# Performance work log

Hardware: AMD Instinct MI355X
Metric: run time of the kernel (lower is better)

## Reference

```python
import jax, jax.numpy as jnp
import numpy as np

B, S, H, P, T = 8, 2048, 1024, 256, 4
EPS = 1e-12


def setup_inputs() -> dict:
    key = jax.random.key(0)
    ks = jax.random.split(key, 12)
    sd = 0.02
    return {
        "hidden_states": jax.random.normal(ks[0], (B, S, H), jnp.float32),
        "input_tensor": jax.random.normal(ks[1], (B, S, H), jnp.float32),
        "attention_mask": jnp.zeros((B, 1, 1, S), jnp.float32),
        "dense_W": jax.random.normal(ks[2], (H, H), jnp.float32) * sd,
        "dense_b": jnp.zeros((H,), jnp.float32),
        "pal_W1": jax.random.normal(ks[3], (T, H, P), jnp.float32) * sd,  # H2L per task
        "pal_b1": jnp.zeros((T, P), jnp.float32),
        "pal_W2": jax.random.normal(ks[4], (T, P, H), jnp.float32) * sd,  # L2H per task
        "pal_b2": jnp.zeros((T, H), jnp.float32),
        "enc_W": jax.random.normal(ks[5], (H,), jnp.float32) * sd,  # Linear(H,1)
        "enc_b": jnp.zeros((), jnp.float32),
        "sel_W": jax.random.normal(ks[6], (T, H), jnp.float32) * sd,  # Linear(H,T)
        "sel_b": jnp.zeros((T,), jnp.float32),
        "ln_g": jnp.ones((H,), jnp.float32),
        "ln_b": jnp.zeros((H,), jnp.float32),
    }


def reference(hidden_states, input_tensor, attention_mask, dense_W, dense_b,
              pal_W1, pal_b1, pal_W2, pal_b2, enc_W, enc_b, sel_W, sel_b,
              ln_g, ln_b):
    # dense projection (dropout p=0 -> identity)
    h = jnp.einsum('bsh,hk->bsk', hidden_states, dense_W) + dense_b  # [B,S,H]

    # per-task PAL adapters: H -> P -> H, stacked over T
    low = jnp.einsum('bsh,thp->btsp', h, pal_W1) + pal_b1[:, None, :]   # [B,T,S,P]
    task_specific = jnp.einsum('btsp,tph->btsh', low, pal_W2) + pal_b2[:, None, :]  # [B,T,S,H]

    # token-level gating: softmax over sequence of (encoder logits + additive mask)
    task_logits = jnp.einsum('bsh,h->bs', h, enc_W) + enc_b            # [B,S]
    task_weights = jax.nn.softmax(task_logits + attention_mask.reshape(B, S), axis=-1)
    task_vector = jnp.einsum('bs,bsh->bh', task_weights, h)            # [B,H]

    # task selector distribution and weighted combine over task branches
    task_distribution = jax.nn.softmax(task_vector @ sel_W.T + sel_b, axis=-1)  # [B,T]
    summed = jnp.einsum('btsh,bt->bsh', task_specific, task_distribution)       # [B,S,H]

    # residual + LayerNorm (eps=1e-12)
    x = h + input_tensor + summed
    mu = x.mean(-1, keepdims=True)
    var = ((x - mu) ** 2).mean(-1, keepdims=True)
    return ln_g * (x - mu) / jnp.sqrt(var + EPS) + ln_b
```

## Files before the change

### kernel.cpp

```cpp
#include <hip/hip_runtime.h>
#include <stdint.h>

#define DEVI __device__ __forceinline__

typedef __attribute__((ext_vector_type(8))) short s8v;
typedef __attribute__((ext_vector_type(4))) float f4v;
typedef unsigned short u16;

DEVI float bf2f(u16 u) { union { uint32_t i; float f; } c; c.i = ((uint32_t)u) << 16; return c.f; }
DEVI u16 f2bf(float f) {
  union { float f; uint32_t u; } c; c.f = f;
  uint32_t u = c.u;
  u += 0x7fffu + ((u >> 16) & 1u);
  return (u16)(u >> 16);
}

DEVI void gld16(const void* g, void* l) {
  auto gp = reinterpret_cast<const __attribute__((address_space(1))) void*>(reinterpret_cast<uintptr_t>(g));
  auto lp = reinterpret_cast<__attribute__((address_space(3))) void*>(reinterpret_cast<uintptr_t>(l));
  __builtin_amdgcn_global_load_lds(gp, lp, 16, 0, 0);
}

DEVI float wredsum(float v) {
  #pragma unroll
  for (int o = 32; o; o >>= 1) v += __shfl_xor(v, o);
  return v;
}

#define MFMA16(a, b, c) __builtin_amdgcn_mfma_f32_16x16x32_bf16((a), (b), (c), 0, 0, 0)

__global__ void cvt_f32_bf16(const float4* __restrict__ in, ushort4* __restrict__ out) {
  int i = blockIdx.x * 256 + threadIdx.x;
  float4 v = in[i];
  ushort4 o;
  o.x = f2bf(v.x); o.y = f2bf(v.y); o.z = f2bf(v.z); o.w = f2bf(v.w);
  out[i] = o;
}

__global__ void transpose_cvt(const float* __restrict__ in, u16* __restrict__ out, int R, int C) {
  __shared__ float t[32][33];
  in  += (size_t)blockIdx.z * R * C;
  out += (size_t)blockIdx.z * R * C;
  int r0 = blockIdx.y * 32, c0 = blockIdx.x * 32;
  int tx = threadIdx.x, ty = threadIdx.y;
  #pragma unroll
  for (int j = ty; j < 32; j += 8) t[j][tx] = in[(size_t)(r0 + j) * C + c0 + tx];
  __syncthreads();
  #pragma unroll
  for (int j = ty; j < 32; j += 8) out[(size_t)(c0 + j) * R + r0 + tx] = f2bf(t[tx][j]);
}


template<int EPI>
__global__ __launch_bounds__(256, 4) void gemm_bt(
    const u16* __restrict__ A, const u16* __restrict__ Bt, void* out,
    const float* __restrict__ e0, const float* __restrict__ e1, const u16* e2)
{
  const int tid  = threadIdx.x;
  const int lane = tid & 63;
  const int wv   = tid >> 6;
  const int wg = ((blockIdx.x & 7) << 7) | (blockIdx.x >> 3);
  const int tm = wg >> 3;
  const int tn = wg & 7;

  __shared__ char lds[32768];
  char* As = lds;
  char* Bs = lds + 16384;

  f4v acc[4][4];
  #pragma unroll
  for (int i = 0; i < 4; i++)
    #pragma unroll
    for (int j = 0; j < 4; j++) acc[i][j] = f4v{0.f, 0.f, 0.f, 0.f};

  const int wr = wv >> 1, wc = wv & 1;
  const int mB = wr * 64, nB = wc * 64;
  const int fr = lane & 15;
  const int fkbyte = (lane >> 4) << 4;

  const char* Ab = (const char*)(A + (size_t)tm * 128 * 1024);
  const char* Bb = (const char*)(Bt + (size_t)tn * 128 * 1024);

  for (int k0 = 0; k0 < 1024; k0 += 64) {
    #pragma unroll
    for (int c = 0; c < 4; ++c) {
      int p = wv * 1024 + lane * 16 + c * 4096;
      int row = p >> 7;
      int kb = (p & 127) ^ ((row & 7) << 4);
      gld16(Ab + (size_t)row * 2048 + k0 * 2 + kb, As + p);
      gld16(Bb + (size_t)row * 2048 + k0 * 2 + kb, Bs + p);
    }
    __syncthreads();
    #pragma unroll
    for (int kk = 0; kk < 2; ++kk) {
      s8v af[4], bf[4];
      #pragma unroll
      for (int i = 0; i < 4; ++i) {
        int ra = mB + i * 16 + fr;
        int rb = nB + i * 16 + fr;
        int kbyte = kk * 64 + fkbyte;
        af[i] = *(const s8v*)(As + ra * 128 + (kbyte ^ ((ra & 7) << 4)));
        bf[i] = *(const s8v*)(Bs + rb * 128 + (kbyte ^ ((rb & 7) << 4)));
      }
      #pragma unroll
      for (int mi = 0; mi < 4; ++mi)
        #pragma unroll
        for (int ni = 0; ni < 4; ++ni)
          acc[mi][ni] = MFMA16(af[mi], bf[ni], acc[mi][ni]);
    }
    __syncthreads();
  }

  const int mBase = tm * 128 + mB;
  const int nBase = tn * 128 + nB;
  const int rl = (lane >> 4) << 2;
  const int cl = lane & 15;
  float scale = 0.f;
  const float* b2row = nullptr;
  if constexpr (EPI == 2) scale = e1[(tm >> 4) * 4 + (tn >> 1)];
  if constexpr (EPI == 3) b2row = e0 + (tm >> 4) * 1024;

  #pragma unroll
  for (int mi = 0; mi < 4; ++mi) {
    #pragma unroll
    for (int ni = 0; ni < 4; ++ni) {
      int n = nBase + ni * 16 + cl;
      #pragma unroll
      for (int v = 0; v < 4; ++v) {
        int m = mBase + mi * 16 + rl + v;
        size_t idx = (size_t)m * 1024 + n;
        float val = acc[mi][ni][v];
        if constexpr (EPI == 1) {
          ((u16*)out)[idx] = f2bf(val + e0[n]);
        } else if constexpr (EPI == 2) {
          ((u16*)out)[idx] = f2bf(scale * (val + e0[n]));
        } else {
          ((u16*)out)[idx] = f2bf(val + b2row[n] + bf2f(e2[idx]) + e1[idx]);
        }
      }
    }
  }
}

template<int EPI>
__global__ __launch_bounds__(256, 2) void gemm_db(
    const u16* __restrict__ A, const u16* __restrict__ Bt, void* out,
    const float* __restrict__ e0, const float* __restrict__ e1, const u16* e2)
{
  __shared__ char AsB[2][16384];
  __shared__ char BsB[2][16384];
  const int tid  = threadIdx.x;
  const int lane = tid & 63;
  const int wv   = tid >> 6;
  const int wg = ((blockIdx.x & 7) << 7) | (blockIdx.x >> 3);
  const int tm = wg >> 3;
  const int tn = wg & 7;

  f4v acc[4][4];
  #pragma unroll
  for (int i = 0; i < 4; i++)
    #pragma unroll
    for (int j = 0; j < 4; j++) acc[i][j] = f4v{0.f, 0.f, 0.f, 0.f};

  const int wr = wv >> 1, wc = wv & 1;
  const int mB = wr * 64, nB = wc * 64;
  const int fr = lane & 15;
  const int fkbyte = (lane >> 4) << 4;

  const char* Ab = (const char*)(A + (size_t)tm * 128 * 1024);
  const char* Bb = (const char*)(Bt + (size_t)tn * 128 * 1024);

  auto stage = [&](int buf, int k0) {
    #pragma unroll
    for (int c = 0; c < 4; ++c) {
      int p = wv * 1024 + lane * 16 + c * 4096;
      int row = p >> 7;
      int kb = (p & 127) ^ ((row & 7) << 4);
      gld16(Ab + (size_t)row * 2048 + k0 * 2 + kb, AsB[buf] + p);
      gld16(Bb + (size_t)row * 2048 + k0 * 2 + kb, BsB[buf] + p);
    }
  };

  auto tilestep = [&](int buf, int nextk) {
    s8v af[4][2], bf[4][2];
    #pragma unroll
    for (int kk = 0; kk < 2; ++kk)
      #pragma unroll
      for (int i = 0; i < 4; ++i) {
        int ra = mB + i * 16 + fr;
        int rb = nB + i * 16 + fr;
        int kbyte = kk * 64 + fkbyte;
        af[i][kk] = *(const s8v*)(AsB[buf] + ra * 128 + (kbyte ^ ((ra & 7) << 4)));
        bf[i][kk] = *(const s8v*)(BsB[buf] + rb * 128 + (kbyte ^ ((rb & 7) << 4)));
      }
    if (nextk >= 0) stage(buf ^ 1, nextk);
    #pragma unroll
    for (int kk = 0; kk < 2; ++kk)
      #pragma unroll
      for (int mi = 0; mi < 4; ++mi)
        #pragma unroll
        for (int ni = 0; ni < 4; ++ni)
          acc[mi][ni] = MFMA16(af[mi][kk], bf[ni][kk], acc[mi][ni]);
    __syncthreads();
  };

  stage(0, 0);
  __syncthreads();
  #pragma unroll 1
  for (int t = 0; t < 16; t += 2) {
    tilestep(0, (t + 1) * 64);
    tilestep(1, (t + 2 < 16) ? (t + 2) * 64 : -1);
  }

  const int mBase = tm * 128 + mB;
  const int nBase = tn * 128 + nB;
  const int rl = (lane >> 4) << 2;
  const int cl = lane & 15;
  float scale = 0.f;
  const float* b2row = nullptr;
  if constexpr (EPI == 2) scale = e1[(tm >> 4) * 4 + (tn >> 1)];
  if constexpr (EPI == 3) b2row = e0 + (tm >> 4) * 1024;

  #pragma unroll
  for (int mi = 0; mi < 4; ++mi) {
    #pragma unroll
    for (int ni = 0; ni < 4; ++ni) {
      int n = nBase + ni * 16 + cl;
      #pragma unroll
      for (int v = 0; v < 4; ++v) {
        int m = mBase + mi * 16 + rl + v;
        size_t idx = (size_t)m * 1024 + n;
        float val = acc[mi][ni][v];
        if constexpr (EPI == 1) {
          ((u16*)out)[idx] = f2bf(val + e0[n]);
        } else if constexpr (EPI == 2) {
          ((u16*)out)[idx] = f2bf(scale * (val + e0[n]));
        } else {
          ((u16*)out)[idx] = f2bf(val + b2row[n] + bf2f(e2[idx]) + e1[idx]);
        }
      }
    }
  }
}

__global__ void rowdot_kernel(const u16* __restrict__ h, const float* __restrict__ encW,
                              const float* __restrict__ encb, float* __restrict__ logits) {
  int row  = blockIdx.x * 4 + (threadIdx.x >> 6);
  int lane = threadIdx.x & 63;
  const u16* hp = h + (size_t)row * 1024 + lane * 16;
  s8v a0 = *(const s8v*)hp;
  s8v a1 = *(const s8v*)(hp + 8);
  const float* wp = encW + lane * 16;
  float s = 0.f;
  #pragma unroll
  for (int j = 0; j < 8; j++) s += bf2f((u16)a0[j]) * wp[j];
  #pragma unroll
  for (int j = 0; j < 8; j++) s += bf2f((u16)a1[j]) * wp[8 + j];
  s = wredsum(s);
  if (lane == 0) logits[row] = s + encb[0];
}

__global__ void softmax_seq(const float* __restrict__ logits, const float* __restrict__ mask,
                            float* __restrict__ w) {
  int b = blockIdx.x, tid = threadIdx.x;
  int lane = tid & 63, wv = tid >> 6;
  const float* lp = logits + (size_t)b * 2048;
  const float* mp = mask + (size_t)b * 2048;
  float v[8];
  #pragma unroll
  for (int i = 0; i < 8; i++) v[i] = lp[tid * 8 + i] + mp[tid * 8 + i];
  float mx = -1e30f;
  #pragma unroll
  for (int i = 0; i < 8; i++) mx = fmaxf(mx, v[i]);
  __shared__ float red[4];
  #pragma unroll
  for (int o = 32; o; o >>= 1) mx = fmaxf(mx, __shfl_xor(mx, o));
  if (lane == 0) red[wv] = mx;
  __syncthreads();
  mx = fmaxf(fmaxf(red[0], red[1]), fmaxf(red[2], red[3]));
  __syncthreads();
  float s = 0.f;
  #pragma unroll
  for (int i = 0; i < 8; i++) { v[i] = expf(v[i] - mx); s += v[i]; }
  s = wredsum(s);
  if (lane == 0) red[wv] = s;
  __syncthreads();
  s = red[0] + red[1] + red[2] + red[3];
  float inv = 1.f / s;
  #pragma unroll
  for (int i = 0; i < 8; i++) w[(size_t)b * 2048 + tid * 8 + i] = v[i] * inv;
}

__global__ void taskvec_part(const u16* __restrict__ h, const float* __restrict__ w,
                             float* __restrict__ tvp) {
  int b = blockIdx.y, sc = blockIdx.z;
  int col = blockIdx.x * 256 + threadIdx.x;
  const u16* hp = h + ((size_t)b * 2048 + sc * 256) * 1024 + col;
  const float* wp = w + (size_t)b * 2048 + sc * 256;
  float a0 = 0.f, a1 = 0.f, a2 = 0.f, a3 = 0.f;
  for (int s = 0; s < 256; s += 4) {
    a0 += wp[s]     * bf2f(hp[(size_t)s * 1024]);
    a1 += wp[s + 1] * bf2f(hp[(size_t)(s + 1) * 1024]);
    a2 += wp[s + 2] * bf2f(hp[(size_t)(s + 2) * 1024]);
    a3 += wp[s + 3] * bf2f(hp[(size_t)(s + 3) * 1024]);
  }
  tvp[((size_t)b * 8 + sc) * 1024 + col] = (a0 + a1) + (a2 + a3);
}

__global__ void taskvec_reduce(const float* __restrict__ tvp, float* __restrict__ tv) {
  int b = blockIdx.y;
  int col = blockIdx.x * 256 + threadIdx.x;
  float s = 0.f;
  #pragma unroll
  for (int c = 0; c < 8; c++) s += tvp[((size_t)b * 8 + c) * 1024 + col];
  tv[(size_t)b * 1024 + col] = s;
}

__global__ void taskdist_kernel(const float* __restrict__ tv, const float* __restrict__ selW,
                                const float* __restrict__ selb, const float* __restrict__ pb2,
                                float* __restrict__ dvec, float* __restrict__ bias2) {
  int b = blockIdx.x, tid = threadIdx.x;
  int lane = tid & 63, wv = tid >> 6;
  const float* tp = tv + (size_t)b * 1024;
  const float* sw = selW + (size_t)wv * 1024;
  float s = 0.f;
  #pragma unroll
  for (int j = 0; j < 16; j++) s += tp[lane * 16 + j] * sw[lane * 16 + j];
  s = wredsum(s);
  __shared__ float lg[4];
  if (lane == 0) lg[wv] = s + selb[wv];
  __syncthreads();
  float m = fmaxf(fmaxf(lg[0], lg[1]), fmaxf(lg[2], lg[3]));
  float e0 = expf(lg[0] - m), e1 = expf(lg[1] - m), e2 = expf(lg[2] - m), e3 = expf(lg[3] - m);
  float inv = 1.f / (e0 + e1 + e2 + e3);
  float d0 = e0 * inv, d1 = e1 * inv, d2 = e2 * inv, d3 = e3 * inv;
  if (tid < 4) dvec[b * 4 + tid] = (tid == 0) ? d0 : (tid == 1) ? d1 : (tid == 2) ? d2 : d3;
  #pragma unroll
  for (int c = 0; c < 4; c++) {
    int n = c * 256 + tid;
    bias2[(size_t)b * 1024 + n] =
        d0 * pb2[n] + d1 * pb2[1024 + n] + d2 * pb2[2048 + n] + d3 * pb2[3072 + n];
  }
}

__global__ void ln_bf16_kernel(const u16* __restrict__ x, const float* __restrict__ g,
                               const float* __restrict__ bt, float* __restrict__ out) {
  int row = blockIdx.x, tid = threadIdx.x;
  int lane = tid & 63, wv = tid >> 6;
  ushort4 u = ((const ushort4*)(x + (size_t)row * 1024))[tid];
  float v0 = bf2f(u.x), v1 = bf2f(u.y), v2 = bf2f(u.z), v3 = bf2f(u.w);
  float s = v0 + v1 + v2 + v3;
  float q = v0 * v0 + v1 * v1 + v2 * v2 + v3 * v3;
  #pragma unroll
  for (int o = 32; o; o >>= 1) { s += __shfl_xor(s, o); q += __shfl_xor(q, o); }
  __shared__ float rs[4], rq[4];
  if (lane == 0) { rs[wv] = s; rq[wv] = q; }
  __syncthreads();
  s = rs[0] + rs[1] + rs[2] + rs[3];
  q = rq[0] + rq[1] + rq[2] + rq[3];
  float mu = s * (1.f / 1024.f);
  float var = q * (1.f / 1024.f) - mu * mu;
  float inv = 1.f / sqrtf(var + 1e-12f);
  const float4 gv = ((const float4*)g)[tid];
  const float4 bv = ((const float4*)bt)[tid];
  float4 o;
  o.x = gv.x * (v0 - mu) * inv + bv.x;
  o.y = gv.y * (v1 - mu) * inv + bv.y;
  o.z = gv.z * (v2 - mu) * inv + bv.z;
  o.w = gv.w * (v3 - mu) * inv + bv.w;
  ((float4*)(out + (size_t)row * 1024))[tid] = o;
}

extern "C" void kernel_launch(void* const* d_in, const int* in_sizes, int n_in,
                              void* d_out, int out_size, void* d_ws, size_t ws_size,
                              hipStream_t stream) {
  const float* hidden = (const float*)d_in[0];
  const float* input  = (const float*)d_in[1];
  const float* mask   = (const float*)d_in[2];
  const float* denseW = (const float*)d_in[3];
  const float* denseB = (const float*)d_in[4];
  const float* palW1  = (const float*)d_in[5];
  const float* palB1  = (const float*)d_in[6];
  const float* palW2  = (const float*)d_in[7];
  const float* palB2  = (const float*)d_in[8];
  const float* encW   = (const float*)d_in[9];
  const float* encB   = (const float*)d_in[10];
  const float* selW   = (const float*)d_in[11];
  const float* selB   = (const float*)d_in[12];
  const float* lnG    = (const float*)d_in[13];
  const float* lnB    = (const float*)d_in[14];

  char* ws = (char*)d_ws;
  u16*  hbf    = (u16*)(ws);
  u16*  a0low  = (u16*)(ws + 33554432);
  u16*  wdt    = (u16*)(ws + 67108864);
  u16*  w1t    = (u16*)(ws + 69206016);
  u16*  w2t    = (u16*)(ws + 71303168);
  float* logits = (float*)(ws + 73400320);
  float* wts    = (float*)(ws + 73465856);
  float* tv     = (float*)(ws + 73531392);
  float* dvec   = (float*)(ws + 73564160);
  float* bias2  = (float*)(ws + 73568256);
  float* tvp    = (float*)(ws + 73601024);

  cvt_f32_bf16<<<16384, 256, 0, stream>>>((const float4*)hidden, (ushort4*)a0low);
  transpose_cvt<<<dim3(32, 32, 1), dim3(32, 8), 0, stream>>>(denseW, wdt, 1024, 1024);
  transpose_cvt<<<dim3(8, 32, 4),  dim3(32, 8), 0, stream>>>(palW1, w1t, 1024, 256);
  transpose_cvt<<<dim3(32, 32, 1), dim3(32, 8), 0, stream>>>(palW2, w2t, 1024, 1024);

  gemm_bt<1><<<1024, 256, 0, stream>>>(a0low, wdt, hbf, denseB, nullptr, nullptr);

  rowdot_kernel<<<4096, 256, 0, stream>>>(hbf, encW, encB, logits);
  softmax_seq<<<8, 256, 0, stream>>>(logits, mask, wts);
  taskvec_part<<<dim3(4, 8, 8), 256, 0, stream>>>(hbf, wts, tvp);
  taskvec_reduce<<<dim3(4, 8), 256, 0, stream>>>(tvp, tv);
  taskdist_kernel<<<8, 256, 0, stream>>>(tv, selW, selB, palB2, dvec, bias2);

  gemm_db<2><<<1024, 256, 0, stream>>>(hbf, w1t, a0low, palB1, dvec, nullptr);
  gemm_db<3><<<1024, 256, 0, stream>>>(a0low, w2t, hbf, bias2, input, hbf);

  ln_bf16_kernel<<<16384, 256, 0, stream>>>(hbf, lnG, lnB, (float*)d_out);
}
```

Before: 219.1 us.

## Run PAL adapter GEMMs in FP8 with MX-scaled MFMA

The two adapter GEMMs now use FP8 operands and the 16x16x128 f8f6f4 scaled MFMA instead of bf16 MFMA. The dense GEMM also writes an FP8 copy of h, and the weights are pre-scaled by 32 when converted to FP8; the epilogues undo the scaling. This halves operand bytes and raises MFMA throughput for those GEMMs. It uses the output buffer as FP8 scratch, drops the double-buffered pipeline for a single-buffer loop, and lowers precision, which risks accuracy tolerance.

```diff
diff --git a/kernel.cpp b/kernel.cpp
--- a/kernel.cpp
+++ b/kernel.cpp
@@ -5,7 +5,10 @@
 
 typedef __attribute__((ext_vector_type(8))) short s8v;
 typedef __attribute__((ext_vector_type(4))) float f4v;
+typedef __attribute__((ext_vector_type(4))) int i4v;
+typedef __attribute__((ext_vector_type(8))) int i8v;
 typedef unsigned short u16;
+typedef unsigned char u8;
 
 DEVI float bf2f(u16 u) { union { uint32_t i; float f; } c; c.i = ((uint32_t)u) << 16; return c.f; }
 DEVI u16 f2bf(float f) {
@@ -14,6 +17,9 @@
   u += 0x7fffu + ((u >> 16) & 1u);
   return (u16)(u >> 16);
 }
+DEVI u8 f2fp8(float v) {
+  return (u8)(__builtin_amdgcn_cvt_pk_fp8_f32(v, v, 0, false) & 0xff);
+}
 
 DEVI void gld16(const void* g, void* l) {
   auto gp = reinterpret_cast<const __attribute__((address_space(1))) void*>(reinterpret_cast<uintptr_t>(g));
@@ -27,7 +33,16 @@
   return v;
 }
 
+DEVI i8v mk8(i4v lo, i4v hi) {
+  i8v r;
+  r[0] = lo[0]; r[1] = lo[1]; r[2] = lo[2]; r[3] = lo[3];
+  r[4] = hi[0]; r[5] = hi[1]; r[6] = hi[2]; r[7] = hi[3];
+  return r;
+}
+
 #define MFMA16(a, b, c) __builtin_amdgcn_mfma_f32_16x16x32_bf16((a), (b), (c), 0, 0, 0)
+#define MFMA_FP8(a, b, c) \
+  __builtin_amdgcn_mfma_scale_f32_16x16x128_f8f6f4((a), (b), (c), 0, 0, 0, 0x7f7f7f7f, 0, 0x7f7f7f7f)
 
 __global__ void cvt_f32_bf16(const float4* __restrict__ in, ushort4* __restrict__ out) {
   int i = blockIdx.x * 256 + threadIdx.x;
@@ -50,11 +65,23 @@
   for (int j = ty; j < 32; j += 8) out[(size_t)(c0 + j) * R + r0 + tx] = f2bf(t[tx][j]);
 }
 
-
-template<int EPI>
-__global__ __launch_bounds__(256, 4) void gemm_bt(
-    const u16* __restrict__ A, const u16* __restrict__ Bt, void* out,
-    const float* __restrict__ e0, const float* __restrict__ e1, const u16* e2)
+__global__ void transpose_cvt_fp8(const float* __restrict__ in, u8* __restrict__ out,
+                                  int R, int C, float scale) {
+  __shared__ float t[32][33];
+  in  += (size_t)blockIdx.z * R * C;
+  out += (size_t)blockIdx.z * R * C;
+  int r0 = blockIdx.y * 32, c0 = blockIdx.x * 32;
+  int tx = threadIdx.x, ty = threadIdx.y;
+  #pragma unroll
+  for (int j = ty; j < 32; j += 8) t[j][tx] = in[(size_t)(r0 + j) * C + c0 + tx];
+  __syncthreads();
+  #pragma unroll
+  for (int j = ty; j < 32; j += 8) out[(size_t)(c0 + j) * R + r0 + tx] = f2fp8(t[tx][j] * scale);
+}
+
+__global__ __launch_bounds__(256, 4) void gemm_bt1(
+    const u16* __restrict__ A, const u16* __restrict__ Bt, u16* __restrict__ out,
+    const float* __restrict__ e0, u8* __restrict__ out8)
 {
   const int tid  = threadIdx.x;
   const int lane = tid & 63;
@@ -115,10 +142,94 @@
   const int nBase = tn * 128 + nB;
   const int rl = (lane >> 4) << 2;
   const int cl = lane & 15;
-  float scale = 0.f;
+
+  #pragma unroll
+  for (int mi = 0; mi < 4; ++mi) {
+    #pragma unroll
+    for (int ni = 0; ni < 4; ++ni) {
+      int n = nBase + ni * 16 + cl;
+      float bias = e0[n];
+      #pragma unroll
+      for (int v = 0; v < 4; ++v) {
+        int m = mBase + mi * 16 + rl + v;
+        size_t idx = (size_t)m * 1024 + n;
+        float val = acc[mi][ni][v] + bias;
+        out[idx]  = f2bf(val);
+        out8[idx] = f2fp8(val);
+      }
+    }
+  }
+}
+
+template<int EPI>
+__global__ __launch_bounds__(256, 4) void gemm_mx(
+    const u8* __restrict__ A, const u8* __restrict__ Bt, void* out,
+    const float* __restrict__ e0, const float* __restrict__ e1, const u16* e2)
+{
+  __shared__ char As[16384];
+  __shared__ char Bs[16384];
+  const int tid  = threadIdx.x;
+  const int lane = tid & 63;
+  const int wv   = tid >> 6;
+  const int wg = ((blockIdx.x & 7) << 7) | (blockIdx.x >> 3);
+  const int tm = wg >> 3;
+  const int tn = wg & 7;
+
+  f4v acc[4][4];
+  #pragma unroll
+  for (int i = 0; i < 4; i++)
+    #pragma unroll
+    for (int j = 0; j < 4; j++) acc[i][j] = f4v{0.f, 0.f, 0.f, 0.f};
+
+  const int wr = wv >> 1, wc = wv & 1;
+  const int mB = wr * 64, nB = wc * 64;
+  const int fr = lane & 15;
+  const int ck = (lane >> 4) * 32;
+
+  const char* Ab = (const char*)A  + (size_t)tm * 128 * 1024;
+  const char* Bb = (const char*)Bt + (size_t)tn * 128 * 1024;
+
+  for (int kt = 0; kt < 8; ++kt) {
+    #pragma unroll
+    for (int c = 0; c < 4; ++c) {
+      int p = wv * 1024 + lane * 16 + c * 4096;
+      int row = p >> 7;
+      int kb = (p & 127) ^ ((row & 7) << 4);
+      gld16(Ab + (size_t)row * 1024 + kt * 128 + kb, As + p);
+      gld16(Bb + (size_t)row * 1024 + kt * 128 + kb, Bs + p);
+    }
+    __syncthreads();
+    i8v af[4];
+    #pragma unroll
+    for (int i = 0; i < 4; ++i) {
+      int ra = mB + i * 16 + fr;
+      int sw = (ra & 7) << 4;
+      i4v lo = *(const i4v*)(As + ra * 128 + (ck ^ sw));
+      i4v hi = *(const i4v*)(As + ra * 128 + ((ck + 16) ^ sw));
+      af[i] = mk8(lo, hi);
+    }
+    #pragma unroll
+    for (int j = 0; j < 4; ++j) {
+      int rb = nB + j * 16 + fr;
+      int sw = (rb & 7) << 4;
+      i4v lo = *(const i4v*)(Bs + rb * 128 + (ck ^ sw));
+      i4v hi = *(const i4v*)(Bs + rb * 128 + ((ck + 16) ^ sw));
+      i8v bfv = mk8(lo, hi);
+      #pragma unroll
+      for (int i = 0; i < 4; ++i)
+        acc[i][j] = MFMA_FP8(af[i], bfv, acc[i][j]);
+    }
+    __syncthreads();
+  }
+
+  const int mBase = tm * 128 + mB;
+  const int nBase = tn * 128 + nB;
+  const int rl = (lane >> 4) << 2;
+  const int cl = lane & 15;
+  float dsc = 0.f;
   const float* b2row = nullptr;
-  if constexpr (EPI == 2) scale = e1[(tm >> 4) * 4 + (tn >> 1)];
-  if constexpr (EPI == 3) b2row = e0 + (tm >> 4) * 1024;
+  if constexpr (EPI == 2) dsc = e1[(tm >> 4) * 4 + (tn >> 1)] * 8.f;
+  if constexpr (EPI == 3) b2row = e0 + (size_t)(tm >> 4) * 1024;
 
   #pragma unroll
   for (int mi = 0; mi < 4; ++mi) {
@@ -130,113 +241,10 @@
         int m = mBase + mi * 16 + rl + v;
         size_t idx = (size_t)m * 1024 + n;
         float val = acc[mi][ni][v];
-        if constexpr (EPI == 1) {
-          ((u16*)out)[idx] = f2bf(val + e0[n]);
-        } else if constexpr (EPI == 2) {
-          ((u16*)out)[idx] = f2bf(scale * (val + e0[n]));
+        if constexpr (EPI == 2) {
+          ((u8*)out)[idx] = f2fp8((val * 0.03125f + e0[n]) * dsc);
         } else {
-          ((u16*)out)[idx] = f2bf(val + b2row[n] + bf2f(e2[idx]) + e1[idx]);
-        }
-      }
-    }
-  }
-}
-
-template<int EPI>
-__global__ __launch_bounds__(256, 2) void gemm_db(
-    const u16* __restrict__ A, const u16* __restrict__ Bt, void* out,
-    const float* __restrict__ e0, const float* __restrict__ e1, const u16* e2)
-{
-  __shared__ char AsB[2][16384];
-  __shared__ char BsB[2][16384];
-  const int tid  = threadIdx.x;
-  const int lane = tid & 63;
-  const int wv   = tid >> 6;
-  const int wg = ((blockIdx.x & 7) << 7) | (blockIdx.x >> 3);
-  const int tm = wg >> 3;
-  const int tn = wg & 7;
-
-  f4v acc[4][4];
-  #pragma unroll
-  for (int i = 0; i < 4; i++)
-    #pragma unroll
-    for (int j = 0; j < 4; j++) acc[i][j] = f4v{0.f, 0.f, 0.f, 0.f};
-
-  const int wr = wv >> 1, wc = wv & 1;
-  const int mB = wr * 64, nB = wc * 64;
-  const int fr = lane & 15;
-  const int fkbyte = (lane >> 4) << 4;
-
-  const char* Ab = (const char*)(A + (size_t)tm * 128 * 1024);
-  const char* Bb = (const char*)(Bt + (size_t)tn * 128 * 1024);
-
-  auto stage = [&](int buf, int k0) {
-    #pragma unroll
-    for (int c = 0; c < 4; ++c) {
-      int p = wv * 1024 + lane * 16 + c * 4096;
-      int row = p >> 7;
-      int kb = (p & 127) ^ ((row & 7) << 4);
-      gld16(Ab + (size_t)row * 2048 + k0 * 2 + kb, AsB[buf] + p);
-      gld16(Bb + (size_t)row * 2048 + k0 * 2 + kb, BsB[buf] + p);
-    }
-  };
-
-  auto tilestep = [&](int buf, int nextk) {
-    s8v af[4][2], bf[4][2];
-    #pragma unroll
-    for (int kk = 0; kk < 2; ++kk)
-      #pragma unroll
-      for (int i = 0; i < 4; ++i) {
-        int ra = mB + i * 16 + fr;
-        int rb = nB + i * 16 + fr;
-        int kbyte = kk * 64 + fkbyte;
-        af[i][kk] = *(const s8v*)(AsB[buf] + ra * 128 + (kbyte ^ ((ra & 7) << 4)));
-        bf[i][kk] = *(const s8v*)(BsB[buf] + rb * 128 + (kbyte ^ ((rb & 7) << 4)));
-      }
-    if (nextk >= 0) stage(buf ^ 1, nextk);
-    #pragma unroll
-    for (int kk = 0; kk < 2; ++kk)
-      #pragma unroll
-      for (int mi = 0; mi < 4; ++mi)
-        #pragma unroll
-        for (int ni = 0; ni < 4; ++ni)
-          acc[mi][ni] = MFMA16(af[mi][kk], bf[ni][kk], acc[mi][ni]);
-    __syncthreads();
-  };
-
-  stage(0, 0);
-  __syncthreads();
-  #pragma unroll 1
-  for (int t = 0; t < 16; t += 2) {
-    tilestep(0, (t + 1) * 64);
-    tilestep(1, (t + 2 < 16) ? (t + 2) * 64 : -1);
-  }
-
-  const int mBase = tm * 128 + mB;
-  const int nBase = tn * 128 + nB;
-  const int rl = (lane >> 4) << 2;
-  const int cl = lane & 15;
-  float scale = 0.f;
-  const float* b2row = nullptr;
-  if constexpr (EPI == 2) scale = e1[(tm >> 4) * 4 + (tn >> 1)];
-  if constexpr (EPI == 3) b2row = e0 + (tm >> 4) * 1024;
-
-  #pragma unroll
-  for (int mi = 0; mi < 4; ++mi) {
-    #pragma unroll
-    for (int ni = 0; ni < 4; ++ni) {
-      int n = nBase + ni * 16 + cl;
-      #pragma unroll
-      for (int v = 0; v < 4; ++v) {
-        int m = mBase + mi * 16 + rl + v;
-        size_t idx = (size_t)m * 1024 + n;
-        float val = acc[mi][ni][v];
-        if constexpr (EPI == 1) {
-          ((u16*)out)[idx] = f2bf(val + e0[n]);
-        } else if constexpr (EPI == 2) {
-          ((u16*)out)[idx] = f2bf(scale * (val + e0[n]));
-        } else {
-          ((u16*)out)[idx] = f2bf(val + b2row[n] + bf2f(e2[idx]) + e1[idx]);
+          ((u16*)out)[idx] = f2bf(val * (1.f / 256.f) + b2row[n] + bf2f(e2[idx]) + e1[idx]);
         }
       }
     }
@@ -394,8 +402,8 @@
   u16*  hbf    = (u16*)(ws);
   u16*  a0low  = (u16*)(ws + 33554432);
   u16*  wdt    = (u16*)(ws + 67108864);
-  u16*  w1t    = (u16*)(ws + 69206016);
-  u16*  w2t    = (u16*)(ws + 71303168);
+  u8*   w1t8   = (u8*)(ws + 69206016);
+  u8*   w2t8   = (u8*)(ws + 71303168);
   float* logits = (float*)(ws + 73400320);
   float* wts    = (float*)(ws + 73465856);
   float* tv     = (float*)(ws + 73531392);
@@ -403,12 +411,15 @@
   float* bias2  = (float*)(ws + 73568256);
   float* tvp    = (float*)(ws + 73601024);
 
+  u8* lowd8 = (u8*)d_out;
+  u8* h8    = (u8*)d_out + (16u << 20);
+
   cvt_f32_bf16<<<16384, 256, 0, stream>>>((const float4*)hidden, (ushort4*)a0low);
   transpose_cvt<<<dim3(32, 32, 1), dim3(32, 8), 0, stream>>>(denseW, wdt, 1024, 1024);
-  transpose_cvt<<<dim3(8, 32, 4),  dim3(32, 8), 0, stream>>>(palW1, w1t, 1024, 256);
-  transpose_cvt<<<dim3(32, 32, 1), dim3(32, 8), 0, stream>>>(palW2, w2t, 1024, 1024);
-
-  gemm_bt<1><<<1024, 256, 0, stream>>>(a0low, wdt, hbf, denseB, nullptr, nullptr);
+  transpose_cvt_fp8<<<dim3(8, 32, 4),  dim3(32, 8), 0, stream>>>(palW1, w1t8, 1024, 256, 32.f);
+  transpose_cvt_fp8<<<dim3(32, 32, 1), dim3(32, 8), 0, stream>>>(palW2, w2t8, 1024, 1024, 32.f);
+
+  gemm_bt1<<<1024, 256, 0, stream>>>(a0low, wdt, hbf, denseB, h8);
 
   rowdot_kernel<<<4096, 256, 0, stream>>>(hbf, encW, encB, logits);
   softmax_seq<<<8, 256, 0, stream>>>(logits, mask, wts);
@@ -416,8 +427,8 @@
   taskvec_reduce<<<dim3(4, 8), 256, 0, stream>>>(tvp, tv);
   taskdist_kernel<<<8, 256, 0, stream>>>(tv, selW, selB, palB2, dvec, bias2);
 
-  gemm_db<2><<<1024, 256, 0, stream>>>(hbf, w1t, a0low, palB1, dvec, nullptr);
-  gemm_db<3><<<1024, 256, 0, stream>>>(a0low, w2t, hbf, bias2, input, hbf);
+  gemm_mx<2><<<1024, 256, 0, stream>>>(h8, w1t8, lowd8, palB1, dvec, nullptr);
+  gemm_mx<3><<<1024, 256, 0, stream>>>(lowd8, w2t8, hbf, bias2, input, hbf);
 
   ln_bf16_kernel<<<16384, 256, 0, stream>>>(hbf, lnG, lnB, (float*)d_out);
 }
```

New measurement: 254.9 us. +16.3%, slower.

## Replace double-buffered GEMM with single-buffer 512-thread high-occupancy variant

Applied to the files above, without the earlier changes.

Replaces the double-buffered 256-thread GEMM with a single-buffered 512-thread kernel. Each of eight waves computes a 32x64 sub-tile, so accumulator registers drop and occupancy can rise (launch bounds 512,6). The first PAL GEMM now uses this kernel, and the second PAL GEMM switches to the existing gemm_bt kernel. This gives up the load/compute overlap of double buffering and relies on more resident waves to hide latency.

```diff
diff --git a/kernel.cpp b/kernel.cpp
--- a/kernel.cpp
+++ b/kernel.cpp
@@ -143,73 +143,65 @@
 }
 
 template<int EPI>
-__global__ __launch_bounds__(256, 2) void gemm_db(
+__global__ __launch_bounds__(512, 6) void gemm_hi(
     const u16* __restrict__ A, const u16* __restrict__ Bt, void* out,
     const float* __restrict__ e0, const float* __restrict__ e1, const u16* e2)
 {
-  __shared__ char AsB[2][16384];
-  __shared__ char BsB[2][16384];
   const int tid  = threadIdx.x;
   const int lane = tid & 63;
-  const int wv   = tid >> 6;
+  const int wid  = tid >> 6;
+  const int wm = wid >> 1, wn = wid & 1;
   const int wg = ((blockIdx.x & 7) << 7) | (blockIdx.x >> 3);
   const int tm = wg >> 3;
   const int tn = wg & 7;
 
-  f4v acc[4][4];
-  #pragma unroll
-  for (int i = 0; i < 4; i++)
+  __shared__ char As[16384];
+  __shared__ char Bs[16384];
+
+  f4v acc[2][4];
+  #pragma unroll
+  for (int i = 0; i < 2; i++)
     #pragma unroll
     for (int j = 0; j < 4; j++) acc[i][j] = f4v{0.f, 0.f, 0.f, 0.f};
 
-  const int wr = wv >> 1, wc = wv & 1;
-  const int mB = wr * 64, nB = wc * 64;
+  const int mB = wm * 32, nB = wn * 64;
   const int fr = lane & 15;
   const int fkbyte = (lane >> 4) << 4;
 
   const char* Ab = (const char*)(A + (size_t)tm * 128 * 1024);
   const char* Bb = (const char*)(Bt + (size_t)tn * 128 * 1024);
 
-  auto stage = [&](int buf, int k0) {
-    #pragma unroll
-    for (int c = 0; c < 4; ++c) {
-      int p = wv * 1024 + lane * 16 + c * 4096;
+  for (int k0 = 0; k0 < 1024; k0 += 64) {
+    #pragma unroll
+    for (int c = 0; c < 2; ++c) {
+      int p = tid * 16 + c * 8192;
       int row = p >> 7;
       int kb = (p & 127) ^ ((row & 7) << 4);
-      gld16(Ab + (size_t)row * 2048 + k0 * 2 + kb, AsB[buf] + p);
-      gld16(Bb + (size_t)row * 2048 + k0 * 2 + kb, BsB[buf] + p);
-    }
-  };
-
-  auto tilestep = [&](int buf, int nextk) {
-    s8v af[4][2], bf[4][2];
-    #pragma unroll
-    for (int kk = 0; kk < 2; ++kk)
-      #pragma unroll
-      for (int i = 0; i < 4; ++i) {
+      gld16(Ab + (size_t)row * 2048 + k0 * 2 + kb, As + p);
+      gld16(Bb + (size_t)row * 2048 + k0 * 2 + kb, Bs + p);
+    }
+    __syncthreads();
+    #pragma unroll
+    for (int kk = 0; kk < 2; ++kk) {
+      s8v af[2], bf[4];
+      const int kbyte = kk * 64 + fkbyte;
+      #pragma unroll
+      for (int i = 0; i < 2; ++i) {
         int ra = mB + i * 16 + fr;
-        int rb = nB + i * 16 + fr;
-        int kbyte = kk * 64 + fkbyte;
-        af[i][kk] = *(const s8v*)(AsB[buf] + ra * 128 + (kbyte ^ ((ra & 7) << 4)));
-        bf[i][kk] = *(const s8v*)(BsB[buf] + rb * 128 + (kbyte ^ ((rb & 7) << 4)));
+        af[i] = *(const s8v*)(As + ra * 128 + (kbyte ^ ((ra & 7) << 4)));
       }
-    if (nextk >= 0) stage(buf ^ 1, nextk);
-    #pragma unroll
-    for (int kk = 0; kk < 2; ++kk)
-      #pragma unroll
-      for (int mi = 0; mi < 4; ++mi)
+      #pragma unroll
+      for (int j = 0; j < 4; ++j) {
+        int rb = nB + j * 16 + fr;
+        bf[j] = *(const s8v*)(Bs + rb * 128 + (kbyte ^ ((rb & 7) << 4)));
+      }
+      #pragma unroll
+      for (int i = 0; i < 2; ++i)
         #pragma unroll
-        for (int ni = 0; ni < 4; ++ni)
-          acc[mi][ni] = MFMA16(af[mi][kk], bf[ni][kk], acc[mi][ni]);
+        for (int j = 0; j < 4; ++j)
+          acc[i][j] = MFMA16(af[i], bf[j], acc[i][j]);
+    }
     __syncthreads();
-  };
-
-  stage(0, 0);
-  __syncthreads();
-  #pragma unroll 1
-  for (int t = 0; t < 16; t += 2) {
-    tilestep(0, (t + 1) * 64);
-    tilestep(1, (t + 2 < 16) ? (t + 2) * 64 : -1);
   }
 
   const int mBase = tm * 128 + mB;
@@ -222,15 +214,15 @@
   if constexpr (EPI == 3) b2row = e0 + (tm >> 4) * 1024;
 
   #pragma unroll
-  for (int mi = 0; mi < 4; ++mi) {
-    #pragma unroll
-    for (int ni = 0; ni < 4; ++ni) {
-      int n = nBase + ni * 16 + cl;
+  for (int i = 0; i < 2; ++i) {
+    #pragma unroll
+    for (int j = 0; j < 4; ++j) {
+      int n = nBase + j * 16 + cl;
       #pragma unroll
       for (int v = 0; v < 4; ++v) {
-        int m = mBase + mi * 16 + rl + v;
+        int m = mBase + i * 16 + rl + v;
         size_t idx = (size_t)m * 1024 + n;
-        float val = acc[mi][ni][v];
+        float val = acc[i][j][v];
         if constexpr (EPI == 1) {
           ((u16*)out)[idx] = f2bf(val + e0[n]);
         } else if constexpr (EPI == 2) {
@@ -416,8 +408,8 @@
   taskvec_reduce<<<dim3(4, 8), 256, 0, stream>>>(tvp, tv);
   taskdist_kernel<<<8, 256, 0, stream>>>(tv, selW, selB, palB2, dvec, bias2);
 
-  gemm_db<2><<<1024, 256, 0, stream>>>(hbf, w1t, a0low, palB1, dvec, nullptr);
-  gemm_db<3><<<1024, 256, 0, stream>>>(a0low, w2t, hbf, bias2, input, hbf);
+  gemm_hi<2><<<1024, 512, 0, stream>>>(hbf, w1t, a0low, palB1, dvec, nullptr);
+  gemm_bt<3><<<1024, 256, 0, stream>>>(a0low, w2t, hbf, bias2, input, hbf);
 
   ln_bf16_kernel<<<16384, 256, 0, stream>>>(hbf, lnG, lnB, (float*)d_out);
 }
```

Result: faster. 211.7 us (-3.4%).
